# Performance work log

Hardware: AMD Instinct MI355X
Metric: run time of the kernel (lower is better)

Reference implementation:

```python
import jax, jax.numpy as jnp
import numpy as np

E, H, C, CE, HID = 500000, 1, 64, 16, 128

def prelu(x, alpha):
    return jnp.where(x >= 0, x, alpha * x)

def setup_inputs() -> dict:
    key = jax.random.key(0)
    k = jax.random.split(key, 8)
    d_in = 2 * C + CE  # 144
    s1 = 1.0 / np.sqrt(d_in)
    s2 = 1.0 / np.sqrt(HID)
    return {
        "x_i": jax.random.normal(k[0], (E, H, C), jnp.float32),
        "x_j": jax.random.normal(k[1], (E, H, C), jnp.float32),
        "edge_attr": jax.random.normal(k[2], (E, H, CE), jnp.float32),
        "W1": jax.random.uniform(k[3], (d_in, HID), jnp.float32, -s1, s1),
        "b1": jax.random.uniform(k[4], (HID,), jnp.float32, -s1, s1),
        "W2": jax.random.uniform(k[5], (HID, C), jnp.float32, -s2, s2),
        "b2": jax.random.uniform(k[6], (C,), jnp.float32, -s2, s2),
        "alpha": jnp.float32(0.25),  # shared PReLU parameter (same module instance reused)
    }

def reference(x_i, x_j, edge_attr, W1, b1, W2, b2, alpha):
    B, Hh, Cc = x_i.shape
    concat = jnp.concatenate([x_i, x_j, edge_attr], axis=-1)       # [E, H, 2C+CE]
    concat = concat.reshape(B * Hh, -1)                             # [E*H, 144]
    h = prelu(concat @ W1 + b1, alpha)                              # [E*H, HID]
    out = prelu(h @ W2 + b2, alpha)                                 # [E*H, C] (dropout=eval identity)
    return out.reshape(B, Hh, Cc)
```

## Files before the change

kernel.cpp:

```cpp
#include <hip/hip_runtime.h>
#include <hip/hip_bf16.h>


#define E_ROWS 500000
#define TILES  15625
#define NBLK   512
#define NWAVES (NBLK * 4)

#define LDW 168

typedef short  bf8_t  __attribute__((ext_vector_type(8)));
typedef float  f32x16 __attribute__((ext_vector_type(16)));

static __device__ __forceinline__ short f2bf(float v) {
    return (short)__builtin_bit_cast(unsigned short, __float2bfloat16(v));
}

__global__ __launch_bounds__(256, 2)
void message_pass_kernel(const float* __restrict__ x_i,
                         const float* __restrict__ x_j,
                         const float* __restrict__ ea,
                         const float* __restrict__ W1,
                         const float* __restrict__ b1,
                         const float* __restrict__ W2,
                         const float* __restrict__ b2,
                         const float* __restrict__ alpha_p,
                         float* __restrict__ out)
{
    __shared__ __align__(16) short sW1[128 * LDW];
    __shared__ __align__(16) short sW2[64 * LDW];

    const int tid = threadIdx.x;

    for (int idx = tid; idx < 128 * LDW; idx += 256) {
        int i = idx & 127, c = idx >> 7;
        float v = 0.f;
        if (c < 144)       v = W1[c * 128 + i];
        else if (c == 144) v = b1[i];
        sW1[i * LDW + c] = f2bf(v);
    }
    for (int idx = tid; idx < 64 * LDW; idx += 256) {
        int i = idx & 63, c = idx >> 6;
        float v = 0.f;
        if (c < 144) {
            int k = (c & ~12) | ((c & 4) << 1) | ((c & 8) >> 1);
            if (k < 128)       v = W2[k * 64 + i];
            else if (k == 128) v = b2[i];
        }
        sW2[i * LDW + c] = f2bf(v);
    }
    __syncthreads();

    const float alpha = alpha_p[0];
    const int lane = tid & 63;
    const int l31  = lane & 31;
    const int g2   = lane >> 5;
    const int wv   = blockIdx.x * 4 + (tid >> 6);

    for (int T = wv; T < TILES; T += NWAVES) {
        const size_t row0 = (size_t)T * 32;
        const float* xi  = x_i + (row0 + l31) * 64 + 8 * g2;
        const float* xj  = x_j + (row0 + l31) * 64 + 8 * g2;
        const float* eaR = ea  + (row0 + l31) * 16 + 8 * g2;

        float4 ld[9][2];
        #pragma unroll
        for (int s = 0; s < 4; ++s) {
            ld[s][0]     = *(const float4*)(xi + 16 * s);
            ld[s][1]     = *(const float4*)(xi + 16 * s + 4);
        }
        #pragma unroll
        for (int s = 0; s < 4; ++s) {
            ld[4 + s][0] = *(const float4*)(xj + 16 * s);
            ld[4 + s][1] = *(const float4*)(xj + 16 * s + 4);
        }
        ld[8][0] = *(const float4*)(eaR);
        ld[8][1] = *(const float4*)(eaR + 4);

        f32x16 acc[4] = {};
        #pragma unroll
        for (int s = 0; s < 9; ++s) {
            bf8_t b;
            b[0] = f2bf(ld[s][0].x); b[1] = f2bf(ld[s][0].y);
            b[2] = f2bf(ld[s][0].z); b[3] = f2bf(ld[s][0].w);
            b[4] = f2bf(ld[s][1].x); b[5] = f2bf(ld[s][1].y);
            b[6] = f2bf(ld[s][1].z); b[7] = f2bf(ld[s][1].w);
            #pragma unroll
            for (int t1 = 0; t1 < 4; ++t1) {
                const bf8_t a = *(const bf8_t*)(sW1 + (32 * t1 + l31) * LDW + 16 * s + 8 * g2);
                acc[t1] = __builtin_amdgcn_mfma_f32_32x32x16_bf16(a, b, acc[t1], 0, 0, 0);
            }
        }
        {
            bf8_t b = {};
            b[0] = (short)(g2 == 0 ? 0x3F80 : 0);
            #pragma unroll
            for (int t1 = 0; t1 < 4; ++t1) {
                const bf8_t a = *(const bf8_t*)(sW1 + (32 * t1 + l31) * LDW + 144 + 8 * g2);
                acc[t1] = __builtin_amdgcn_mfma_f32_32x32x16_bf16(a, b, acc[t1], 0, 0, 0);
            }
        }

        f32x16 acc2[2] = {};
        #pragma unroll
        for (int s = 0; s < 8; ++s) {
            const int t = s >> 1, rb = (s & 1) * 8;
            bf8_t a;
            #pragma unroll
            for (int e = 0; e < 8; ++e) {
                float v = acc[t][rb + e];
                v = fmaxf(v, 0.f) + alpha * fminf(v, 0.f);
                a[e] = f2bf(v);
            }
            #pragma unroll
            for (int t2 = 0; t2 < 2; ++t2) {
                const bf8_t bb = *(const bf8_t*)(sW2 + (32 * t2 + l31) * LDW + 16 * s + 8 * g2);
                acc2[t2] = __builtin_amdgcn_mfma_f32_32x32x16_bf16(a, bb, acc2[t2], 0, 0, 0);
            }
        }
        {
            bf8_t a = {};
            a[0] = (short)(g2 == 0 ? 0x3F80 : 0);
            #pragma unroll
            for (int t2 = 0; t2 < 2; ++t2) {
                const bf8_t bb = *(const bf8_t*)(sW2 + (32 * t2 + l31) * LDW + 128 + 8 * g2);
                acc2[t2] = __builtin_amdgcn_mfma_f32_32x32x16_bf16(a, bb, acc2[t2], 0, 0, 0);
            }
        }

        float* op = out + row0 * 64;
        #pragma unroll
        for (int t2 = 0; t2 < 2; ++t2) {
            #pragma unroll
            for (int r = 0; r < 16; ++r) {
                const int m = (r & 3) + 8 * (r >> 2) + 4 * g2;
                float v = acc2[t2][r];
                v = fmaxf(v, 0.f) + alpha * fminf(v, 0.f);
                op[(size_t)m * 64 + 32 * t2 + l31] = v;
            }
        }
    }
}

extern "C" void kernel_launch(void* const* d_in, const int* in_sizes, int n_in,
                              void* d_out, int out_size, void* d_ws, size_t ws_size,
                              hipStream_t stream) {
    const float* x_i  = (const float*)d_in[0];
    const float* x_j  = (const float*)d_in[1];
    const float* ea   = (const float*)d_in[2];
    const float* W1   = (const float*)d_in[3];
    const float* b1   = (const float*)d_in[4];
    const float* W2   = (const float*)d_in[5];
    const float* b2   = (const float*)d_in[6];
    const float* alph = (const float*)d_in[7];
    message_pass_kernel<<<NBLK, 256, 0, stream>>>(x_i, x_j, ea, W1, b1, W2, b2, alph,
                                                  (float*)d_out);
}
```

Baseline: 423.9 us.

## Double-buffer input tile loads in registers and fold bias2 into accumulator init

Splits the per-tile work into load and compute lambdas and ping-pongs between two register buffers, so the next tile's global loads are issued before the current tile's MFMA work. The second-layer bias is now used to initialise the accumulators, which drops one MFMA pair per tile. The LDS strides are shrunk for the W1 and W2 tiles. The extra 72 floats of register buffering may raise VGPR pressure under launch_bounds(256,2).

```diff
diff --git a/kernel.cpp b/kernel.cpp
--- a/kernel.cpp
+++ b/kernel.cpp
@@ -7,7 +7,8 @@
 #define NBLK   512
 #define NWAVES (NBLK * 4)
 
-#define LDW 168
+#define LDW1 152
+#define LDW2 136
 
 typedef short  bf8_t  __attribute__((ext_vector_type(8)));
 typedef float  f32x16 __attribute__((ext_vector_type(16)));
@@ -27,27 +28,24 @@
                          const float* __restrict__ alpha_p,
                          float* __restrict__ out)
 {
-    __shared__ __align__(16) short sW1[128 * LDW];
-    __shared__ __align__(16) short sW2[64 * LDW];
+    __shared__ __align__(16) short sW1[128 * LDW1 + 16];
+    __shared__ __align__(16) short sW2[64 * LDW2];
 
     const int tid = threadIdx.x;
 
-    for (int idx = tid; idx < 128 * LDW; idx += 256) {
+    for (int idx = tid; idx < 128 * LDW1; idx += 256) {
         int i = idx & 127, c = idx >> 7;
         float v = 0.f;
         if (c < 144)       v = W1[c * 128 + i];
         else if (c == 144) v = b1[i];
-        sW1[i * LDW + c] = f2bf(v);
+        sW1[i * LDW1 + c] = f2bf(v);
     }
-    for (int idx = tid; idx < 64 * LDW; idx += 256) {
+    if (tid < 16) sW1[128 * LDW1 + tid] = 0;
+    for (int idx = tid; idx < 64 * LDW2; idx += 256) {
         int i = idx & 63, c = idx >> 6;
-        float v = 0.f;
-        if (c < 144) {
-            int k = (c & ~12) | ((c & 4) << 1) | ((c & 8) >> 1);
-            if (k < 128)       v = W2[k * 64 + i];
-            else if (k == 128) v = b2[i];
-        }
-        sW2[i * LDW + c] = f2bf(v);
+        int k = (c & ~12) | ((c & 4) << 1) | ((c & 8) >> 1);
+        float v = (k < 128) ? W2[k * 64 + i] : 0.f;
+        sW2[i * LDW2 + c] = f2bf(v);
     }
     __syncthreads();
 
@@ -57,25 +55,27 @@
     const int g2   = lane >> 5;
     const int wv   = blockIdx.x * 4 + (tid >> 6);
 
-    for (int T = wv; T < TILES; T += NWAVES) {
+    const float bias2_0 = b2[l31];
+    const float bias2_1 = b2[32 + l31];
+
+    auto load_tile = [&](float4 (&ld)[9][2], int T) {
         const size_t row0 = (size_t)T * 32;
-        const float* xi  = x_i + (row0 + l31) * 64 + 8 * g2;
-        const float* xj  = x_j + (row0 + l31) * 64 + 8 * g2;
-        const float* eaR = ea  + (row0 + l31) * 16 + 8 * g2;
-
-        float4 ld[9][2];
+        const float* xi = x_i + (row0 + l31) * 64 + 8 * g2;
+        const float* xj = x_j + (row0 + l31) * 64 + 8 * g2;
+        const float* er = ea  + (row0 + l31) * 16 + 8 * g2;
         #pragma unroll
         for (int s = 0; s < 4; ++s) {
             ld[s][0]     = *(const float4*)(xi + 16 * s);
             ld[s][1]     = *(const float4*)(xi + 16 * s + 4);
-        }
-        #pragma unroll
-        for (int s = 0; s < 4; ++s) {
             ld[4 + s][0] = *(const float4*)(xj + 16 * s);
             ld[4 + s][1] = *(const float4*)(xj + 16 * s + 4);
         }
-        ld[8][0] = *(const float4*)(eaR);
-        ld[8][1] = *(const float4*)(eaR + 4);
+        ld[8][0] = *(const float4*)(er);
+        ld[8][1] = *(const float4*)(er + 4);
+    };
+
+    auto compute_tile = [&](const float4 (&ld)[9][2], int T) {
+        const size_t row0 = (size_t)T * 32;
 
         f32x16 acc[4] = {};
         #pragma unroll
@@ -87,7 +87,7 @@
             b[6] = f2bf(ld[s][1].z); b[7] = f2bf(ld[s][1].w);
             #pragma unroll
             for (int t1 = 0; t1 < 4; ++t1) {
-                const bf8_t a = *(const bf8_t*)(sW1 + (32 * t1 + l31) * LDW + 16 * s + 8 * g2);
+                const bf8_t a = *(const bf8_t*)(sW1 + (32 * t1 + l31) * LDW1 + 16 * s + 8 * g2);
                 acc[t1] = __builtin_amdgcn_mfma_f32_32x32x16_bf16(a, b, acc[t1], 0, 0, 0);
             }
         }
@@ -96,12 +96,14 @@
             b[0] = (short)(g2 == 0 ? 0x3F80 : 0);
             #pragma unroll
             for (int t1 = 0; t1 < 4; ++t1) {
-                const bf8_t a = *(const bf8_t*)(sW1 + (32 * t1 + l31) * LDW + 144 + 8 * g2);
+                const bf8_t a = *(const bf8_t*)(sW1 + (32 * t1 + l31) * LDW1 + 144 + 8 * g2);
                 acc[t1] = __builtin_amdgcn_mfma_f32_32x32x16_bf16(a, b, acc[t1], 0, 0, 0);
             }
         }
 
-        f32x16 acc2[2] = {};
+        f32x16 acc2[2];
+        #pragma unroll
+        for (int r = 0; r < 16; ++r) { acc2[0][r] = bias2_0; acc2[1][r] = bias2_1; }
         #pragma unroll
         for (int s = 0; s < 8; ++s) {
             const int t = s >> 1, rb = (s & 1) * 8;
@@ -114,16 +116,7 @@
             }
             #pragma unroll
             for (int t2 = 0; t2 < 2; ++t2) {
-                const bf8_t bb = *(const bf8_t*)(sW2 + (32 * t2 + l31) * LDW + 16 * s + 8 * g2);
-                acc2[t2] = __builtin_amdgcn_mfma_f32_32x32x16_bf16(a, bb, acc2[t2], 0, 0, 0);
-            }
-        }
-        {
-            bf8_t a = {};
-            a[0] = (short)(g2 == 0 ? 0x3F80 : 0);
-            #pragma unroll
-            for (int t2 = 0; t2 < 2; ++t2) {
-                const bf8_t bb = *(const bf8_t*)(sW2 + (32 * t2 + l31) * LDW + 128 + 8 * g2);
+                const bf8_t bb = *(const bf8_t*)(sW2 + (32 * t2 + l31) * LDW2 + 16 * s + 8 * g2);
                 acc2[t2] = __builtin_amdgcn_mfma_f32_32x32x16_bf16(a, bb, acc2[t2], 0, 0, 0);
             }
         }
@@ -139,6 +132,21 @@
                 op[(size_t)m * 64 + 32 * t2 + l31] = v;
             }
         }
+    };
+
+    float4 bufA[9][2], bufB[9][2];
+    int T = wv;
+    load_tile(bufA, T);
+    for (;;) {
+        int T1 = T + NWAVES;
+        if (T1 >= TILES) { compute_tile(bufA, T); break; }
+        load_tile(bufB, T1);
+        compute_tile(bufA, T);
+        int T2 = T1 + NWAVES;
+        if (T2 >= TILES) { compute_tile(bufB, T1); break; }
+        load_tile(bufA, T2);
+        compute_tile(bufB, T1);
+        T = T2;
     }
 }
 
```

Result: slower. 504.7 us (+19.1%).
